# Optimization experiments

Hardware: AMD Instinct MI355X
Metric: run time of the kernel (lower is better)

Reference implementation:

```python
import jax, jax.numpy as jnp
import numpy as np

N_NODES = 100000
N_EDGES = 800000
HIDDEN = 128
BN_EPS = 1e-5


def setup_inputs() -> dict:
    key = jax.random.key(0)
    k1, k2, k3 = jax.random.split(key, 3)
    x = jax.random.normal(k1, (N_NODES, HIDDEN), dtype=jnp.float32)
    edge_index = jax.random.randint(k2, (2, N_EDGES), 0, N_NODES, dtype=jnp.int64)
    # Glorot-style init for the GCN linear weight
    W = jax.random.normal(k3, (HIDDEN, HIDDEN), dtype=jnp.float32) / np.sqrt(HIDDEN)
    b = jnp.zeros((HIDDEN,), dtype=jnp.float32)
    gamma = jnp.ones((HIDDEN,), dtype=jnp.float32)
    beta = jnp.zeros((HIDDEN,), dtype=jnp.float32)
    return {"x": x, "edge_index": edge_index, "W": W, "b": b, "gamma": gamma, "beta": beta}


def reference(x, edge_index, W, b, gamma, beta):
    N = x.shape[0]
    xw = x @ W  # [N, d] linear transform first (PyG order)

    # add self-loops
    loops = jnp.arange(N, dtype=edge_index.dtype)
    row = jnp.concatenate([edge_index[0], loops])  # source
    col = jnp.concatenate([edge_index[1], loops])  # target

    # symmetric degree normalization on A~ = A + I
    deg = jax.ops.segment_sum(jnp.ones_like(col, dtype=x.dtype), col, num_segments=N)
    dinv = jax.lax.rsqrt(jnp.maximum(deg, 1.0))  # deg >= 1 due to self-loops
    norm = dinv[row] * dinv[col]  # [E+N]

    # gather -> scale -> scatter-add aggregation
    msgs = xw[row] * norm[:, None]  # [E+N, d]
    agg = jax.ops.segment_sum(msgs, col, num_segments=N) + b  # [N, d]

    # BatchNorm1d (batch statistics, biased variance) + ReLU; Dropout is identity (eval)
    mean = jnp.mean(agg, axis=0)
    var = jnp.var(agg, axis=0)
    h = (agg - mean) * jax.lax.rsqrt(var + BN_EPS) * gamma + beta
    return jax.nn.relu(h)
```

## Files before the change

kernel.cpp:

```cpp
#include <hip/hip_runtime.h>
#include <cstddef>

#define HIDDEN 128
#define BN_EPS 1e-5f
#define KS 136
#define BKT 64

typedef __attribute__((ext_vector_type(8))) short short8;
typedef __attribute__((ext_vector_type(4))) float float4v;
typedef __attribute__((ext_vector_type(4))) unsigned uint4v;

__device__ inline unsigned bf16_rne(float f) {
    unsigned u = __float_as_uint(f);
    return (u + 0x7fff + ((u >> 16) & 1)) >> 16;
}
__device__ inline unsigned pack2_bf16(float a, float b) {
    return bf16_rne(a) | (bf16_rne(b) << 16);
}

__global__ __launch_bounds__(256) void k_front(const float* __restrict__ x,
                                               const float* __restrict__ W,
                                               unsigned short* __restrict__ xus,
                                               const int* __restrict__ col,
                                               const int* __restrict__ row,
                                               int* __restrict__ cnt, int* bucket,
                                               int N, int E, int GB, int CB) {
    __shared__ unsigned short lA[128 * KS];
    __shared__ unsigned short lB[128 * KS];
    int bid = blockIdx.x;
    int tid = threadIdx.x;
    int m2 = 2 * (GB < CB ? GB : CB);
    bool isGemm;
    int rid;
    if (bid < m2) {
        isGemm = (bid & 1);
        rid = bid >> 1;
    } else {
        isGemm = (GB > CB);
        rid = (m2 >> 1) + (bid - m2);
    }

    if (!isGemm) {
        int base = (rid * 256 + tid) * 4;
        if (base + 3 < E) {
            int4 c = *(const int4*)&col[base];
            int4 r = *(const int4*)&row[base];
            int p0 = atomicAdd(&cnt[c.x], 1);
            int p1 = atomicAdd(&cnt[c.y], 1);
            int p2 = atomicAdd(&cnt[c.z], 1);
            int p3 = atomicAdd(&cnt[c.w], 1);
            if (p0 < BKT) bucket[(size_t)c.x * BKT + p0] = r.x;
            if (p1 < BKT) bucket[(size_t)c.y * BKT + p1] = r.y;
            if (p2 < BKT) bucket[(size_t)c.z * BKT + p2] = r.z;
            if (p3 < BKT) bucket[(size_t)c.w * BKT + p3] = r.w;
        } else {
            for (int k = 0; k < 4; ++k) {
                int e = base + k;
                if (e < E) {
                    int c = col[e];
                    int r = row[e];
                    int p = atomicAdd(&cnt[c], 1);
                    if (p < BKT) bucket[(size_t)c * BKT + p] = r;
                }
            }
        }
        return;
    }

    int row0 = rid * 128;
    int wv = tid >> 6;
    int lane = tid & 63;
    int l15 = lane & 15;
    int lq = lane >> 4;

    for (int it = 0; it < 16; ++it) {
        int idx4 = it * 256 + tid;
        int m = idx4 >> 5, c4 = idx4 & 31;
        int grow = row0 + m;
        float4 v = make_float4(0.f, 0.f, 0.f, 0.f);
        if (grow < N) v = ((const float4*)x)[(size_t)grow * 32 + c4];
        uint2 pk;
        pk.x = pack2_bf16(v.x, v.y);
        pk.y = pack2_bf16(v.z, v.w);
        *(uint2*)&lA[m * KS + c4 * 4] = pk;
    }
    for (int it = 0; it < 16; ++it) {
        int idx4 = it * 256 + tid;
        int k = idx4 >> 5, n4 = idx4 & 31;
        float4 v = ((const float4*)W)[(size_t)k * 32 + n4];
        int n = n4 * 4;
        lB[(n + 0) * KS + k] = (unsigned short)bf16_rne(v.x);
        lB[(n + 1) * KS + k] = (unsigned short)bf16_rne(v.y);
        lB[(n + 2) * KS + k] = (unsigned short)bf16_rne(v.z);
        lB[(n + 3) * KS + k] = (unsigned short)bf16_rne(v.w);
    }
    __syncthreads();

    float4v acc[2][8];
#pragma unroll
    for (int i = 0; i < 2; ++i)
#pragma unroll
        for (int j = 0; j < 8; ++j) acc[i][j] = (float4v){0.f, 0.f, 0.f, 0.f};

#pragma unroll
    for (int kc = 0; kc < 4; ++kc) {
        int ko = kc * 32 + lq * 8;
        short8 a0 = *(const short8*)&lA[(wv * 32 + l15) * KS + ko];
        short8 a1 = *(const short8*)&lA[(wv * 32 + 16 + l15) * KS + ko];
        short8 bfr[8];
#pragma unroll
        for (int nt = 0; nt < 8; ++nt)
            bfr[nt] = *(const short8*)&lB[(nt * 16 + l15) * KS + ko];
#pragma unroll
        for (int nt = 0; nt < 8; ++nt) {
            acc[0][nt] = __builtin_amdgcn_mfma_f32_16x16x32_bf16(a0, bfr[nt], acc[0][nt], 0, 0, 0);
            acc[1][nt] = __builtin_amdgcn_mfma_f32_16x16x32_bf16(a1, bfr[nt], acc[1][nt], 0, 0, 0);
        }
    }

    __syncthreads();

#pragma unroll
    for (int mt = 0; mt < 2; ++mt) {
#pragma unroll
        for (int reg = 0; reg < 4; ++reg) {
            int rl = wv * 32 + mt * 16 + lq * 4 + reg;
#pragma unroll
            for (int nt = 0; nt < 8; ++nt)
                lA[rl * KS + nt * 16 + l15] = (unsigned short)bf16_rne(acc[mt][nt][reg]);
        }
    }
    __syncthreads();

    for (int it = 0; it < 8; ++it) {
        int idx = it * 256 + tid;
        int r = idx >> 4, c16 = idx & 15;
        int grow = row0 + r;
        if (grow < N) {
            uint4v v = *(const uint4v*)&lA[r * KS + c16 * 8];
            *((uint4v*)(xus + (size_t)grow * 128) + c16) = v;
        }
    }
}

__global__ __launch_bounds__(256) void k_gather(const unsigned* __restrict__ xu,
                                                const int* __restrict__ cnt,
                                                const float* __restrict__ b,
                                                unsigned* aggsrc,
                                                float* __restrict__ bn, int N) {
    int tid = threadIdx.x;
    int lane = tid & 63;
    int w = (blockIdx.x * 256 + tid) >> 6;
    int nw = (gridDim.x * 256) >> 6;
    float2 bb = ((const float2*)b)[lane];
    float2 s = make_float2(0.f, 0.f), qq = make_float2(0.f, 0.f);

    const int* bkt = (const int*)aggsrc;

    int i = w;
    int deg = 0;
    unsigned uself = 0;
    int pf[16];
#pragma unroll
    for (int k = 0; k < 16; ++k) pf[k] = 0;
    if (i < N) {
        deg = cnt[i];
        uself = xu[(size_t)i * 64 + lane];
        const int4* bp = (const int4*)(bkt + (size_t)i * BKT);
        int4 q0 = bp[0], q1 = bp[1], q2 = bp[2], q3 = bp[3];
        pf[0] = q0.x; pf[1] = q0.y; pf[2]  = q0.z; pf[3]  = q0.w;
        pf[4] = q1.x; pf[5] = q1.y; pf[6]  = q1.z; pf[7]  = q1.w;
        pf[8] = q2.x; pf[9] = q2.y; pf[10] = q2.z; pf[11] = q2.w;
        pf[12] = q3.x; pf[13] = q3.y; pf[14] = q3.z; pf[15] = q3.w;
    }

    while (i < N) {
        int inext = i + nw;
        int ndeg = 0;
        unsigned nself = 0;
        int npf[16];
#pragma unroll
        for (int k = 0; k < 16; ++k) npf[k] = 0;
        if (inext < N) {
            ndeg = cnt[inext];
            nself = xu[(size_t)inext * 64 + lane];
            const int4* bp = (const int4*)(bkt + (size_t)inext * BKT);
            int4 q0 = bp[0], q1 = bp[1], q2 = bp[2], q3 = bp[3];
            npf[0] = q0.x; npf[1] = q0.y; npf[2]  = q0.z; npf[3]  = q0.w;
            npf[4] = q1.x; npf[5] = q1.y; npf[6]  = q1.z; npf[7]  = q1.w;
            npf[8] = q2.x; npf[9] = q2.y; npf[10] = q2.z; npf[11] = q2.w;
            npf[12] = q3.x; npf[13] = q3.y; npf[14] = q3.z; npf[15] = q3.w;
        }

        int d = __builtin_amdgcn_readfirstlane(deg);
        if (d > BKT) d = BKT;
        float di = rsqrtf((float)(d + 1));
        float ax = __uint_as_float(uself << 16) * di;
        float ay = __uint_as_float(uself & 0xffff0000u) * di;

        if (d > 0) {
            int rks[8];
            unsigned u[8];
            float ds[8];
#pragma unroll
            for (int k = 0; k < 8; ++k) rks[k] = (k < d) ? pf[k] : pf[0];
#pragma unroll
            for (int k = 0; k < 8; ++k) u[k] = xu[(size_t)rks[k] * 64 + lane];
#pragma unroll
            for (int k = 0; k < 8; ++k) ds[k] = rsqrtf((float)(cnt[rks[k]] + 1));
#pragma unroll
            for (int k = 0; k < 8; ++k) {
                unsigned uu = (k < d) ? u[k] : 0u;
                ax = fmaf(__uint_as_float(uu << 16), ds[k], ax);
                ay = fmaf(__uint_as_float(uu & 0xffff0000u), ds[k], ay);
            }
        }
        if (d > 8) {
            int rks[8];
            unsigned u[8];
            float ds[8];
#pragma unroll
            for (int k = 0; k < 8; ++k) rks[k] = (8 + k < d) ? pf[8 + k] : pf[0];
#pragma unroll
            for (int k = 0; k < 8; ++k) u[k] = xu[(size_t)rks[k] * 64 + lane];
#pragma unroll
            for (int k = 0; k < 8; ++k) ds[k] = rsqrtf((float)(cnt[rks[k]] + 1));
#pragma unroll
            for (int k = 0; k < 8; ++k) {
                unsigned uu = (8 + k < d) ? u[k] : 0u;
                ax = fmaf(__uint_as_float(uu << 16), ds[k], ax);
                ay = fmaf(__uint_as_float(uu & 0xffff0000u), ds[k], ay);
            }
        }
        if (d > 16) {
            const int* bp = bkt + (size_t)i * BKT;
            int j = 16;
            for (; j + 8 <= d; j += 8) {
                int rr[8];
                unsigned u[8];
                float ds[8];
#pragma unroll
                for (int k = 0; k < 8; ++k) rr[k] = bp[j + k];
#pragma unroll
                for (int k = 0; k < 8; ++k) u[k] = xu[(size_t)rr[k] * 64 + lane];
#pragma unroll
                for (int k = 0; k < 8; ++k) ds[k] = rsqrtf((float)(cnt[rr[k]] + 1));
#pragma unroll
                for (int k = 0; k < 8; ++k) {
                    ax = fmaf(__uint_as_float(u[k] << 16), ds[k], ax);
                    ay = fmaf(__uint_as_float(u[k] & 0xffff0000u), ds[k], ay);
                }
            }
            if (j < d) {
                int last = d - 1;
                int rr[7];
                unsigned u[7];
                float ds[7];
#pragma unroll
                for (int k = 0; k < 7; ++k) {
                    int jk = j + k;
                    rr[k] = bp[jk < d ? jk : last];
                }
#pragma unroll
                for (int k = 0; k < 7; ++k) u[k] = xu[(size_t)rr[k] * 64 + lane];
#pragma unroll
                for (int k = 0; k < 7; ++k) ds[k] = rsqrtf((float)(cnt[rr[k]] + 1));
#pragma unroll
                for (int k = 0; k < 7; ++k) {
                    unsigned uu = (j + k < d) ? u[k] : 0u;
                    ax = fmaf(__uint_as_float(uu << 16), ds[k], ax);
                    ay = fmaf(__uint_as_float(uu & 0xffff0000u), ds[k], ay);
                }
            }
        }

        float ox = fmaf(ax, di, bb.x);
        float oy = fmaf(ay, di, bb.y);
        aggsrc[(size_t)i * 64 + lane] = pack2_bf16(ox, oy);
        s.x += ox;
        s.y += oy;
        qq.x = fmaf(ox, ox, qq.x);
        qq.y = fmaf(oy, oy, qq.y);

        i = inext;
        deg = ndeg;
        uself = nself;
#pragma unroll
        for (int k = 0; k < 16; ++k) pf[k] = npf[k];
    }

    __shared__ float ssum[HIDDEN];
    __shared__ float ssq[HIDDEN];
    if (tid < HIDDEN) { ssum[tid] = 0.f; ssq[tid] = 0.f; }
    __syncthreads();
    atomicAdd(&ssum[2 * lane],     s.x);
    atomicAdd(&ssum[2 * lane + 1], s.y);
    atomicAdd(&ssq[2 * lane],      qq.x);
    atomicAdd(&ssq[2 * lane + 1],  qq.y);
    __syncthreads();
    if (tid < HIDDEN) {
        atomicAdd(&bn[tid],          ssum[tid]);
        atomicAdd(&bn[HIDDEN + tid], ssq[tid]);
    }
}

__global__ __launch_bounds__(256) void k_apply(const unsigned* __restrict__ agg,
                                               float* __restrict__ out,
                                               const float* __restrict__ bn,
                                               const float* __restrict__ gamma,
                                               const float* __restrict__ beta,
                                               int total8, float invN) {
    __shared__ float sc[HIDDEN], sh[HIDDEN];
    int tid = threadIdx.x;
    if (tid < HIDDEN) {
        float mean = bn[tid] * invN;
        float var = bn[HIDDEN + tid] * invN - mean * mean;
        float inv = rsqrtf(var + BN_EPS);
        float g = gamma[tid] * inv;
        sc[tid] = g;
        sh[tid] = beta[tid] - mean * g;
    }
    __syncthreads();
    int idx = blockIdx.x * 256 + tid;
    if (idx < total8) {
        uint2 u = ((const uint2*)agg)[idx];
        int c = (idx & 31) * 4;
        float4 v;
        v.x = __uint_as_float(u.x << 16);
        v.y = __uint_as_float(u.x & 0xffff0000u);
        v.z = __uint_as_float(u.y << 16);
        v.w = __uint_as_float(u.y & 0xffff0000u);
        v.x = fmaxf(fmaf(v.x, sc[c],     sh[c]),     0.f);
        v.y = fmaxf(fmaf(v.y, sc[c + 1], sh[c + 1]), 0.f);
        v.z = fmaxf(fmaf(v.z, sc[c + 2], sh[c + 2]), 0.f);
        v.w = fmaxf(fmaf(v.w, sc[c + 3], sh[c + 3]), 0.f);
        ((float4*)out)[idx] = v;
    }
}

extern "C" void kernel_launch(void* const* d_in, const int* in_sizes, int n_in,
                              void* d_out, int out_size, void* d_ws, size_t ws_size,
                              hipStream_t stream) {
    const float* x     = (const float*)d_in[0];
    const int*   edges = (const int*)d_in[1];
    const float* W     = (const float*)d_in[2];
    const float* b     = (const float*)d_in[3];
    const float* gamma = (const float*)d_in[4];
    const float* beta  = (const float*)d_in[5];
    float* out = (float*)d_out;

    int N = in_sizes[0] / HIDDEN;
    int E = in_sizes[1] / 2;
    const int* row = edges;
    const int* col = edges + E;

    char* p = (char*)d_ws;
    unsigned* xu  = (unsigned*)p; p += (size_t)N * 64 * sizeof(unsigned);
    unsigned* agg = (unsigned*)p; p += (size_t)N * 64 * sizeof(unsigned);
    int*   cnt    = (int*)p;   p += (size_t)N * sizeof(int);
    float* bn     = (float*)p; p += 256 * sizeof(float);

    size_t zbytes = (size_t)N * sizeof(int) + 256 * sizeof(float);

    int GB = (N + 127) / 128;
    int CB = (E + 1023) / 1024;

    dim3 blk(256);
    hipMemsetAsync(cnt, 0, zbytes, stream);
    k_front<<<dim3(GB + CB), blk, 0, stream>>>(x, W, (unsigned short*)xu, col, row,
                                               cnt, (int*)agg, N, E, GB, CB);
    k_gather<<<dim3(2048), blk, 0, stream>>>(xu, cnt, b, agg, bn, N);
    int total8 = N * 32;
    k_apply<<<dim3((total8 + 255) / 256), blk, 0, stream>>>(agg, out, bn, gamma, beta,
                                                            total8, 1.0f / (float)N);
}
```

Measured before the change: 262.6 us.

## Load GEMM A operand directly from global and drop lA shared buffer

```diff
diff --git a/kernel.cpp b/kernel.cpp
--- a/kernel.cpp
+++ b/kernel.cpp
@@ -17,15 +17,22 @@
 __device__ inline unsigned pack2_bf16(float a, float b) {
     return bf16_rne(a) | (bf16_rne(b) << 16);
 }
-
-__global__ __launch_bounds__(256) void k_front(const float* __restrict__ x,
-                                               const float* __restrict__ W,
-                                               unsigned short* __restrict__ xus,
-                                               const int* __restrict__ col,
-                                               const int* __restrict__ row,
-                                               int* __restrict__ cnt, int* bucket,
-                                               int N, int E, int GB, int CB) {
-    __shared__ unsigned short lA[128 * KS];
+__device__ inline short8 pack8_bf16(float4 a, float4 b) {
+    union { unsigned u[4]; short8 s; } t;
+    t.u[0] = pack2_bf16(a.x, a.y);
+    t.u[1] = pack2_bf16(a.z, a.w);
+    t.u[2] = pack2_bf16(b.x, b.y);
+    t.u[3] = pack2_bf16(b.z, b.w);
+    return t.s;
+}
+
+__global__ __launch_bounds__(256, 4) void k_front(const float* __restrict__ x,
+                                                  const float* __restrict__ W,
+                                                  unsigned short* __restrict__ xus,
+                                                  const int* __restrict__ col,
+                                                  const int* __restrict__ row,
+                                                  int* __restrict__ cnt, int* bucket,
+                                                  int N, int E, int GB, int CB) {
     __shared__ unsigned short lB[128 * KS];
     int bid = blockIdx.x;
     int tid = threadIdx.x;
@@ -41,28 +48,12 @@
     }
 
     if (!isGemm) {
-        int base = (rid * 256 + tid) * 4;
-        if (base + 3 < E) {
-            int4 c = *(const int4*)&col[base];
-            int4 r = *(const int4*)&row[base];
-            int p0 = atomicAdd(&cnt[c.x], 1);
-            int p1 = atomicAdd(&cnt[c.y], 1);
-            int p2 = atomicAdd(&cnt[c.z], 1);
-            int p3 = atomicAdd(&cnt[c.w], 1);
-            if (p0 < BKT) bucket[(size_t)c.x * BKT + p0] = r.x;
-            if (p1 < BKT) bucket[(size_t)c.y * BKT + p1] = r.y;
-            if (p2 < BKT) bucket[(size_t)c.z * BKT + p2] = r.z;
-            if (p3 < BKT) bucket[(size_t)c.w * BKT + p3] = r.w;
-        } else {
-            for (int k = 0; k < 4; ++k) {
-                int e = base + k;
-                if (e < E) {
-                    int c = col[e];
-                    int r = row[e];
-                    int p = atomicAdd(&cnt[c], 1);
-                    if (p < BKT) bucket[(size_t)c * BKT + p] = r;
-                }
-            }
+        int e = rid * 256 + tid;
+        if (e < E) {
+            int c = col[e];
+            int r = row[e];
+            int p = atomicAdd(&cnt[c], 1);
+            if (p < BKT) bucket[(size_t)c * BKT + p] = r;
         }
         return;
     }
@@ -73,17 +64,6 @@
     int l15 = lane & 15;
     int lq = lane >> 4;
 
-    for (int it = 0; it < 16; ++it) {
-        int idx4 = it * 256 + tid;
-        int m = idx4 >> 5, c4 = idx4 & 31;
-        int grow = row0 + m;
-        float4 v = make_float4(0.f, 0.f, 0.f, 0.f);
-        if (grow < N) v = ((const float4*)x)[(size_t)grow * 32 + c4];
-        uint2 pk;
-        pk.x = pack2_bf16(v.x, v.y);
-        pk.y = pack2_bf16(v.z, v.w);
-        *(uint2*)&lA[m * KS + c4 * 4] = pk;
-    }
     for (int it = 0; it < 16; ++it) {
         int idx4 = it * 256 + tid;
         int k = idx4 >> 5, n4 = idx4 & 31;
@@ -102,11 +82,21 @@
 #pragma unroll
         for (int j = 0; j < 8; ++j) acc[i][j] = (float4v){0.f, 0.f, 0.f, 0.f};
 
+    int r0g = row0 + wv * 32 + l15;
+    int r1g = r0g + 16;
+    const float4 z4 = make_float4(0.f, 0.f, 0.f, 0.f);
+
 #pragma unroll
     for (int kc = 0; kc < 4; ++kc) {
         int ko = kc * 32 + lq * 8;
-        short8 a0 = *(const short8*)&lA[(wv * 32 + l15) * KS + ko];
-        short8 a1 = *(const short8*)&lA[(wv * 32 + 16 + l15) * KS + ko];
+        const float4* xr0 = (const float4*)x + (size_t)r0g * 32 + (ko >> 2);
+        const float4* xr1 = (const float4*)x + (size_t)r1g * 32 + (ko >> 2);
+        float4 v00 = (r0g < N) ? xr0[0] : z4;
+        float4 v01 = (r0g < N) ? xr0[1] : z4;
+        float4 v10 = (r1g < N) ? xr1[0] : z4;
+        float4 v11 = (r1g < N) ? xr1[1] : z4;
+        short8 a0 = pack8_bf16(v00, v01);
+        short8 a1 = pack8_bf16(v10, v11);
         short8 bfr[8];
 #pragma unroll
         for (int nt = 0; nt < 8; ++nt)
@@ -127,7 +117,7 @@
             int rl = wv * 32 + mt * 16 + lq * 4 + reg;
 #pragma unroll
             for (int nt = 0; nt < 8; ++nt)
-                lA[rl * KS + nt * 16 + l15] = (unsigned short)bf16_rne(acc[mt][nt][reg]);
+                lB[rl * KS + nt * 16 + l15] = (unsigned short)bf16_rne(acc[mt][nt][reg]);
         }
     }
     __syncthreads();
@@ -137,7 +127,7 @@
         int r = idx >> 4, c16 = idx & 15;
         int grow = row0 + r;
         if (grow < N) {
-            uint4v v = *(const uint4v*)&lA[r * KS + c16 * 8];
+            uint4v v = *(const uint4v*)&lB[r * KS + c16 * 8];
             *((uint4v*)(xus + (size_t)grow * 128) + c16) = v;
         }
     }
@@ -363,7 +353,7 @@
     size_t zbytes = (size_t)N * sizeof(int) + 256 * sizeof(float);
 
     int GB = (N + 127) / 128;
-    int CB = (E + 1023) / 1024;
+    int CB = (E + 255) / 256;
 
     dim3 blk(256);
     hipMemsetAsync(cnt, 0, zbytes, stream);
```

Result: no change. 261.3 us (median of 2 runs) (-0.5%).
